# Kernel optimization log

Measured on AMD Instinct MI355X. Metric: run time of the kernel, lower is better.

The kernel has to match this reference:

```python
import jax, jax.numpy as jnp
import numpy as np

MAP_CHANNEL_WEIGHT = 50.0
PATCH = 3  # unfold kernel size and stride (stride == kernel -> non-overlapping)


def setup_inputs() -> dict:
    key = jax.random.key(0)
    k1, k2, k3, k4 = jax.random.split(key, 4)
    style_resp = jax.random.normal(k1, (1, 256, 256, 256), dtype=jnp.float32)
    style_map = jax.random.uniform(k2, (1, 3, 1024, 1024), dtype=jnp.float32)
    output_map = jax.random.uniform(k3, (1, 3, 1024, 1024), dtype=jnp.float32)
    model_resp = jax.random.normal(k4, (1, 256, 256, 256), dtype=jnp.float32)
    return {"style_resp": style_resp, "style_map": style_map,
            "output_map": output_map, "model_resp": model_resp}


def _avg_pool(x, d):
    # x: (N, C, H, W) -> AvgPool2d((d, d)) with default stride = kernel
    n, c, h, w = x.shape
    return x.reshape(n, c, h // d, d, w // d, d).mean(axis=(3, 5))


def _unfold(x):
    # x: (C, H, W) -> (C*3*3, P) matching torch.nn.Unfold((3,3), stride=3)
    # block layout along dim 0 is (C, kh, kw); patches are row-major.
    c, h, w = x.shape
    nh = (h - PATCH) // PATCH + 1
    nw = (w - PATCH) // PATCH + 1
    x = x[:, : nh * PATCH, : nw * PATCH].reshape(c, nh, PATCH, nw, PATCH)
    x = x.transpose(0, 2, 4, 1, 3)  # (C, kh, kw, nh, nw)
    return x.reshape(c * PATCH * PATCH, nh * nw)


def reference(style_resp, style_map, output_map, model_resp):
    # --- init-time precomputation (faithful to __init__) ---
    channel_count = style_resp.shape[0]  # original code uses dim 0 (batch) here
    patch_height = style_resp.shape[2]
    down = style_map.shape[2] // patch_height
    style_map_down = _avg_pool(style_map, down)
    output_map_down = _avg_pool(output_map, down)
    sr = jnp.concatenate(
        [style_resp, MAP_CHANNEL_WEIGHT * style_map_down * channel_count], axis=1)
    style_patches = _unfold(sr[0])                      # (D, P)
    style_norm_inv = 1.0 / jnp.linalg.norm(style_patches, axis=0)  # (P,)

    # --- loss(model_response) ---
    img = jnp.concatenate(
        [model_resp, MAP_CHANNEL_WEIGHT * output_map_down * channel_count], axis=1)
    img_patches = _unfold(img[0])                       # (D, P)
    img_norm_inv = 1.0 / jnp.linalg.norm(img_patches, axis=0)      # (P,)

    # Faithful to original: sim = ((img^T @ style) * img_norm[j]).T * style_norm[j]
    # => C[i, j] = <img_j, style_i> * img_norm_inv[i] * style_norm_inv[j]
    sim = jnp.einsum('di,dj->ij', style_patches, img_patches)  # (P, P): <style_i, img_j>
    sim = sim * img_norm_inv[:, None] * style_norm_inv[None, :]
    nearest = jnp.argmax(sim, axis=1)                   # (P,)

    matched = style_patches[:, nearest]                 # (D, P)
    loss = jnp.mean((img_patches - matched) ** 2)
    return loss
```

## Files before the change

kernel.cpp:

```cpp
#include <hip/hip_runtime.h>
#include <float.h>
#include <math.h>

#define D_REAL 2331
#define D_PAD  2336
#define DQ     2304
#define N_REAL 7225
#define N_PAD  7296
#define JTILES 57
#define ITILES 57
#define STILES 15

typedef __attribute__((ext_vector_type(8))) short bf16x8_t;
typedef __attribute__((ext_vector_type(4))) float f32x4_t;
typedef __attribute__((ext_vector_type(8))) int   v8i_t;
typedef __attribute__((ext_vector_type(4))) int   v4i_t;

__device__ __forceinline__ unsigned short f2bf(float x) {
    union { float f; unsigned int u; } v; v.f = x;
    unsigned int r = v.u + 0x7FFFu + ((v.u >> 16) & 1u);
    return (unsigned short)(r >> 16);
}
__device__ __forceinline__ float bflo(unsigned int u) {
    union { unsigned int x; float f; } v; v.x = u << 16; return v.f;
}
__device__ __forceinline__ float bfhi(unsigned int u) {
    union { unsigned int x; float f; } v; v.x = u & 0xFFFF0000u; return v.f;
}

#define GLOAD_LDS16(g, l) __builtin_amdgcn_global_load_lds( \
    (const __attribute__((address_space(1))) void*)(g),     \
    (__attribute__((address_space(3))) void*)(l), 16, 0, 0)

__global__ __launch_bounds__(256) void build_all(
        const float* __restrict__ respS, const float* __restrict__ respI,
        const float* __restrict__ mapS,  const float* __restrict__ mapI,
        unsigned short* __restrict__ PbS, unsigned short* __restrict__ PbI,
        unsigned char* __restrict__ PqS, unsigned char* __restrict__ PqI) {
    const int mat = blockIdx.y;
    unsigned short* Pb = mat ? PbI : PbS;
    const int bx = blockIdx.x;
    if (bx < 6120) {
        const float* resp = mat ? respI : respS;
        unsigned char* Pq = mat ? PqI : PqS;
        __shared__ float slab[5 * 768];
        const int u  = bx / 72;
        const int d0 = (bx - u * 72) * 32;
        const int c0 = d0 / 9;
        const int cN = (d0 + 31) / 9 - c0 + 1;
        const int total4 = cN * 192;
        for (int idx = threadIdx.x; idx < total4; idx += 256) {
            int cc = idx / 192;
            int rem = idx - cc * 192;
            *(float4*)&slab[cc * 768 + rem * 4] =
                *(const float4*)&resp[(((size_t)(c0 + cc)) << 16)
                                      + ((size_t)(3 * u) << 8) + rem * 4];
        }
        __syncthreads();
        const int dl16 = threadIdx.x & 15;
        const int de = d0 + 2 * dl16, dq = de + 1;
        const int ce = de / 9, re = de - ce * 9, pe = re / 3, qe = re - pe * 3;
        const int co = dq / 9, ro = dq - co * 9, po = ro / 3, qo = ro - po * 3;
        const int base_e = (ce - c0) * 768 + pe * 256 + qe;
        const int base_o = (co - c0) * 768 + po * 256 + qo;
        const int v0 = threadIdx.x >> 4;
        for (int v = v0; v < 85; v += 16) {
            float x0 = slab[base_e + 3 * v];
            float x1 = slab[base_o + 3 * v];
            size_t row = (size_t)(u * 85 + v);
            *(unsigned int*)&Pb[row * D_PAD + de] =
                (unsigned int)f2bf(x0) | ((unsigned int)f2bf(x1) << 16);
            int pk = __builtin_amdgcn_cvt_pk_fp8_f32(x0, x1, 0, false);
            *(unsigned short*)&Pq[row * DQ + de] = (unsigned short)pk;
        }
    } else {
        const float* map = mat ? mapI : mapS;
        int t = (bx - 6120) * 256 + threadIdx.x;
        int n = t >> 5, dm = t & 31;
        if (n >= N_REAL) return;
        float val = 0.f;
        if (dm < 27) {
            int u = n / 85, v = n - u * 85;
            int ch = dm / 9, r9 = dm - ch * 9, p = r9 / 3, q = r9 - p * 3;
            const float* mp = map + ((size_t)ch << 20)
                                  + ((size_t)((3 * u + p) * 4) << 10)
                                  + (size_t)((3 * v + q) * 4);
            float s = 0.f;
            #pragma unroll
            for (int a = 0; a < 4; a++)
                #pragma unroll
                for (int b = 0; b < 4; b++) s += mp[a * 1024 + b];
            val = 3.125f * s;
        }
        Pb[(size_t)n * D_PAD + 2304 + dm] = f2bf(val);
    }
}

__global__ __launch_bounds__(256) void col_norms(const unsigned short* __restrict__ Sb,
                                                 float* __restrict__ sinv) {
    int n = blockIdx.x * 4 + (threadIdx.x >> 6);
    int lane = threadIdx.x & 63;
    const uint4* sp = (const uint4*)(Sb + (size_t)n * D_PAD);
    float s = 0.f;
    for (int k = lane; k < D_PAD / 8; k += 64) {
        uint4 a = sp[k];
        float x0 = bflo(a.x), x1 = bfhi(a.x), x2 = bflo(a.y), x3 = bfhi(a.y);
        float x4 = bflo(a.z), x5 = bfhi(a.z), x6 = bflo(a.w), x7 = bfhi(a.w);
        s = fmaf(x0, x0, s); s = fmaf(x1, x1, s);
        s = fmaf(x2, x2, s); s = fmaf(x3, x3, s);
        s = fmaf(x4, x4, s); s = fmaf(x5, x5, s);
        s = fmaf(x6, x6, s); s = fmaf(x7, x7, s);
    }
    #pragma unroll
    for (int off = 32; off > 0; off >>= 1) s += __shfl_xor(s, off);
    if (lane == 0) sinv[n] = (n < N_REAL) ? rsqrtf(s) : 0.f;
}

__global__ __launch_bounds__(256) void gemm_argmax(
        const unsigned char* __restrict__ Sq, const unsigned char* __restrict__ Iq,
        const unsigned short* __restrict__ Sb, const unsigned short* __restrict__ Ib,
        const float* __restrict__ sinv,
        float* __restrict__ pval, int* __restrict__ pidx) {
    const int lb = blockIdx.x;
    const int sup = lb >> 4, win = lb & 15;
    const int it4 = (sup / STILES) * 4 + (win & 3);
    const int jt4 = (sup % STILES) * 4 + (win >> 2);
    if (it4 >= ITILES || jt4 >= JTILES) return;
    const int i0 = it4 * 128, j0 = jt4 * 128;

    __shared__ __align__(16) unsigned char Af[2][128][128];
    __shared__ __align__(16) unsigned char Bf[2][128][128];
    const int tid = threadIdx.x;
    const int L = tid & 63, w = tid >> 6;
    const int m = L & 15, q = L >> 4;
    const int wi = (w >> 1) * 64, wj = (w & 1) * 64;

    f32x4_t acc[4][4];
    #pragma unroll
    for (int a = 0; a < 4; a++)
        #pragma unroll
        for (int b = 0; b < 4; b++) acc[a][b] = (f32x4_t){0.f, 0.f, 0.f, 0.f};

    const int rl = L >> 3;
    const int ck = (L & 7) ^ rl;
    const unsigned char* gqa = Sq + (size_t)(i0 + w * 32 + rl) * DQ + (ck << 4);
    const unsigned char* gqb = Iq + (size_t)(j0 + w * 32 + rl) * DQ + (ck << 4);

    const int clo = ((((q << 1))     ^ (m & 7)) << 4);
    const int chi = ((((q << 1) | 1) ^ (m & 7)) << 4);

    unsigned short (*At)[32] = (unsigned short(*)[32])&Af[0][0][0];
    unsigned short (*Bt)[32] = (unsigned short(*)[32])&Bf[0][0][0];
    const int rl2 = L >> 2;
    const int ck2 = (L & 3) ^ ((rl2 >> 1) & 3);
    const unsigned short* gta = Sb + (size_t)(i0 + w * 32 + rl2) * D_PAD + 2304 + (ck2 << 3);
    const unsigned short* gtb = Ib + (size_t)(j0 + w * 32 + rl2) * D_PAD + 2304 + (ck2 << 3);
    const int cht = (q ^ ((m >> 1) & 3)) << 3;

#define PREFETCH_Q(buf) {                                     \
    GLOAD_LDS16(gqa,             &Af[buf][w * 32     ][0]);   \
    GLOAD_LDS16(gqa +  8 * DQ,   &Af[buf][w * 32 +  8][0]);   \
    GLOAD_LDS16(gqa + 16 * DQ,   &Af[buf][w * 32 + 16][0]);   \
    GLOAD_LDS16(gqa + 24 * DQ,   &Af[buf][w * 32 + 24][0]);   \
    GLOAD_LDS16(gqb,             &Bf[buf][w * 32     ][0]);   \
    GLOAD_LDS16(gqb +  8 * DQ,   &Bf[buf][w * 32 +  8][0]);   \
    GLOAD_LDS16(gqb + 16 * DQ,   &Bf[buf][w * 32 + 16][0]);   \
    GLOAD_LDS16(gqb + 24 * DQ,   &Bf[buf][w * 32 + 24][0]);   \
    gqa += 128; gqb += 128; }

#define COMPUTE_Q(buf) {                                                   \
    v8i_t aq[4], bq[4];                                                    \
    _Pragma("unroll")                                                      \
    for (int mi = 0; mi < 4; mi++) {                                       \
        v4i_t lo = *(const v4i_t*)&Af[buf][wi + mi * 16 + m][clo];         \
        v4i_t hi = *(const v4i_t*)&Af[buf][wi + mi * 16 + m][chi];         \
        aq[mi] = __builtin_shufflevector(lo, hi, 0, 1, 2, 3, 4, 5, 6, 7);  \
    }                                                                      \
    _Pragma("unroll")                                                      \
    for (int nj = 0; nj < 4; nj++) {                                       \
        v4i_t lo = *(const v4i_t*)&Bf[buf][wj + nj * 16 + m][clo];         \
        v4i_t hi = *(const v4i_t*)&Bf[buf][wj + nj * 16 + m][chi];         \
        bq[nj] = __builtin_shufflevector(lo, hi, 0, 1, 2, 3, 4, 5, 6, 7);  \
    }                                                                      \
    _Pragma("unroll")                                                      \
    for (int mi = 0; mi < 4; mi++)                                         \
        _Pragma("unroll")                                                  \
        for (int nj = 0; nj < 4; nj++)                                     \
            acc[mi][nj] = __builtin_amdgcn_mfma_scale_f32_16x16x128_f8f6f4(\
                aq[mi], bq[nj], acc[mi][nj], 0, 0, 0, 0x7F, 0, 0x7F); }

    PREFETCH_Q(0)
    for (int p = 0; p < 8; p++) {
        __syncthreads();
        PREFETCH_Q(1)
        __builtin_amdgcn_sched_barrier(0);
        COMPUTE_Q(0)
        __syncthreads();
        PREFETCH_Q(0)
        __builtin_amdgcn_sched_barrier(0);
        COMPUTE_Q(1)
    }
    __syncthreads();
    PREFETCH_Q(1)
    __builtin_amdgcn_sched_barrier(0);
    COMPUTE_Q(0)
    __syncthreads();
    {
        GLOAD_LDS16(gta,                      &At[w * 32][0]);
        GLOAD_LDS16(gta + (size_t)16 * D_PAD, &At[w * 32 + 16][0]);
        GLOAD_LDS16(gtb,                      &Bt[w * 32][0]);
        GLOAD_LDS16(gtb + (size_t)16 * D_PAD, &Bt[w * 32 + 16][0]);
    }
    __builtin_amdgcn_sched_barrier(0);
    COMPUTE_Q(1)
    __syncthreads();
    {
        bf16x8_t af[4], bfr[4];
        #pragma unroll
        for (int mi = 0; mi < 4; mi++)
            af[mi] = *(const bf16x8_t*)&At[wi + mi * 16 + m][cht];
        #pragma unroll
        for (int nj = 0; nj < 4; nj++)
            bfr[nj] = *(const bf16x8_t*)&Bt[wj + nj * 16 + m][cht];
        #pragma unroll
        for (int mi = 0; mi < 4; mi++)
            #pragma unroll
            for (int nj = 0; nj < 4; nj++)
                acc[mi][nj] = __builtin_amdgcn_mfma_f32_16x16x32_bf16(
                    af[mi], bfr[nj], acc[mi][nj], 0, 0, 0);
    }
#undef PREFETCH_Q
#undef COMPUTE_Q

    float sjv[4];
    #pragma unroll
    for (int nj = 0; nj < 4; nj++) sjv[nj] = sinv[j0 + wj + nj * 16 + m];
    #pragma unroll
    for (int mi = 0; mi < 4; mi++) {
        #pragma unroll
        for (int r = 0; r < 4; r++) {
            float best = -INFINITY; int bidx = 0x7fffffff;
            #pragma unroll
            for (int nj = 0; nj < 4; nj++) {
                int j = j0 + wj + nj * 16 + m;
                float v = (j < N_REAL) ? acc[mi][nj][r] * sjv[nj] : -INFINITY;
                if (v > best) { best = v; bidx = j; }
            }
            #pragma unroll
            for (int off = 1; off < 16; off <<= 1) {
                float ov = __shfl_xor(best, off);
                int   oi = __shfl_xor(bidx, off);
                if (ov > best || (ov == best && oi < bidx)) { best = ov; bidx = oi; }
            }
            if (m == 0) {
                int i = i0 + wi + mi * 16 + q * 4 + r;
                pval[(size_t)jt4 * N_PAD + i] = best;
                pidx[(size_t)jt4 * N_PAD + i] = bidx;
            }
        }
    }
}

__global__ __launch_bounds__(256) void loss_kernel(
        const unsigned short* __restrict__ Ib, const unsigned short* __restrict__ Sb,
        const float* __restrict__ pval, const int* __restrict__ pidx,
        double* __restrict__ partial) {
    __shared__ float wsum[4];
    __shared__ int sjn;
    const int n = blockIdx.x;
    if (threadIdx.x < 64) {
        float v = -INFINITY; int id = 0x7fffffff;
        if (threadIdx.x < JTILES) {
            v  = pval[(size_t)threadIdx.x * N_PAD + n];
            id = pidx[(size_t)threadIdx.x * N_PAD + n];
        }
        #pragma unroll
        for (int off = 32; off > 0; off >>= 1) {
            float ov = __shfl_xor(v, off);
            int   oi = __shfl_xor(id, off);
            if (ov > v || (ov == v && oi < id)) { v = ov; id = oi; }
        }
        if (threadIdx.x == 0) sjn = id;
    }
    __syncthreads();
    const int jn = sjn;
    const uint4* ip = (const uint4*)(Ib + (size_t)n  * D_PAD);
    const uint4* sp = (const uint4*)(Sb + (size_t)jn * D_PAD);
    float s = 0.f;
    for (int k = threadIdx.x; k < D_PAD / 8; k += 256) {
        uint4 a = ip[k], b = sp[k];
        float d0 = bflo(a.x) - bflo(b.x), d1 = bfhi(a.x) - bfhi(b.x);
        float d2 = bflo(a.y) - bflo(b.y), d3 = bfhi(a.y) - bfhi(b.y);
        float d4 = bflo(a.z) - bflo(b.z), d5 = bfhi(a.z) - bfhi(b.z);
        float d6 = bflo(a.w) - bflo(b.w), d7 = bfhi(a.w) - bfhi(b.w);
        s = fmaf(d0, d0, s); s = fmaf(d1, d1, s);
        s = fmaf(d2, d2, s); s = fmaf(d3, d3, s);
        s = fmaf(d4, d4, s); s = fmaf(d5, d5, s);
        s = fmaf(d6, d6, s); s = fmaf(d7, d7, s);
    }
    #pragma unroll
    for (int off = 32; off > 0; off >>= 1) s += __shfl_xor(s, off);
    int lane = threadIdx.x & 63, wv = threadIdx.x >> 6;
    if (lane == 0) wsum[wv] = s;
    __syncthreads();
    if (threadIdx.x == 0) {
        partial[n] = (double)wsum[0] + (double)wsum[1]
                   + (double)wsum[2] + (double)wsum[3];
    }
}

__global__ __launch_bounds__(256) void finalize(const double* __restrict__ partial,
                                                float* __restrict__ out) {
    __shared__ double ws[4];
    double s = 0.0;
    for (int i = threadIdx.x; i < N_REAL; i += 256) s += partial[i];
    #pragma unroll
    for (int off = 32; off > 0; off >>= 1) s += __shfl_xor(s, off);
    int lane = threadIdx.x & 63, wv = threadIdx.x >> 6;
    if (lane == 0) ws[wv] = s;
    __syncthreads();
    if (threadIdx.x == 0) {
        double t = ws[0] + ws[1] + ws[2] + ws[3];
        out[0] = (float)(t / (double)((long long)D_REAL * N_REAL));
    }
}

extern "C" void kernel_launch(void* const* d_in, const int* in_sizes, int n_in,
                              void* d_out, int out_size, void* d_ws, size_t ws_size,
                              hipStream_t stream) {
    const float* style_resp = (const float*)d_in[0];
    const float* style_map  = (const float*)d_in[1];
    const float* output_map = (const float*)d_in[2];
    const float* model_resp = (const float*)d_in[3];
    float* out = (float*)d_out;

    unsigned short* Sb = (unsigned short*)d_ws;
    unsigned short* Ib = Sb + (size_t)D_PAD * N_PAD;
    unsigned char*  Sq = (unsigned char*)(Ib + (size_t)D_PAD * N_PAD);
    unsigned char*  Iq = Sq + (size_t)DQ * N_PAD;
    float* sinv     = (float*)(Iq + (size_t)DQ * N_PAD);
    float* pval     = sinv + N_PAD;
    int*   pidx     = (int*)(pval + (size_t)JTILES * N_PAD);
    double* partial = (double*)(pidx + (size_t)JTILES * N_PAD);

    build_all<<<dim3(6120 + 904, 2), 256, 0, stream>>>(
        style_resp, model_resp, style_map, output_map, Sb, Ib, Sq, Iq);

    col_norms<<<N_PAD / 4, 256, 0, stream>>>(Sb, sinv);

    gemm_argmax<<<STILES * STILES * 16, 256, 0, stream>>>(Sq, Iq, Sb, Ib, sinv, pval, pidx);

    loss_kernel<<<N_REAL, 256, 0, stream>>>(Ib, Sb, pval, pidx, partial);
    finalize<<<1, 256, 0, stream>>>(partial, out);
}
```

Baseline: 425.0 us.

## Load fp8 A operand directly into registers, halve LDS, target two blocks per CU

The style-patch (A) operand of the fp8 GEMM is now loaded straight from global memory into registers in MFMA fragment layout, double-buffered in registers, and no longer staged through shared memory. Only B goes through LDS, which halves LDS use, and launch bounds now ask for two blocks per CU. The map pooling loop also switches to float4 loads. The trade-off is more register pressure, plus A fragment loads that are less coalesced, with each lane reading 32 bytes from separate rows and no cross-wave reuse of A.

```diff
diff --git a/kernel.cpp b/kernel.cpp
--- a/kernel.cpp
+++ b/kernel.cpp
@@ -87,9 +87,10 @@
                                   + (size_t)((3 * v + q) * 4);
             float s = 0.f;
             #pragma unroll
-            for (int a = 0; a < 4; a++)
-                #pragma unroll
-                for (int b = 0; b < 4; b++) s += mp[a * 1024 + b];
+            for (int a = 0; a < 4; a++) {
+                float4 r = *(const float4*)(mp + a * 1024);
+                s += (r.x + r.y) + (r.z + r.w);
+            }
             val = 3.125f * s;
         }
         Pb[(size_t)n * D_PAD + 2304 + dm] = f2bf(val);
@@ -116,7 +117,7 @@
     if (lane == 0) sinv[n] = (n < N_REAL) ? rsqrtf(s) : 0.f;
 }
 
-__global__ __launch_bounds__(256) void gemm_argmax(
+__global__ __launch_bounds__(256, 2) void gemm_argmax(
         const unsigned char* __restrict__ Sq, const unsigned char* __restrict__ Iq,
         const unsigned short* __restrict__ Sb, const unsigned short* __restrict__ Ib,
         const float* __restrict__ sinv,
@@ -128,7 +129,6 @@
     if (it4 >= ITILES || jt4 >= JTILES) return;
     const int i0 = it4 * 128, j0 = jt4 * 128;
 
-    __shared__ __align__(16) unsigned char Af[2][128][128];
     __shared__ __align__(16) unsigned char Bf[2][128][128];
     const int tid = threadIdx.x;
     const int L = tid & 63, w = tid >> 6;
@@ -143,39 +143,43 @@
 
     const int rl = L >> 3;
     const int ck = (L & 7) ^ rl;
-    const unsigned char* gqa = Sq + (size_t)(i0 + w * 32 + rl) * DQ + (ck << 4);
     const unsigned char* gqb = Iq + (size_t)(j0 + w * 32 + rl) * DQ + (ck << 4);
 
     const int clo = ((((q << 1))     ^ (m & 7)) << 4);
     const int chi = ((((q << 1) | 1) ^ (m & 7)) << 4);
 
-    unsigned short (*At)[32] = (unsigned short(*)[32])&Af[0][0][0];
-    unsigned short (*Bt)[32] = (unsigned short(*)[32])&Bf[0][0][0];
+    const unsigned char* gA[4];
+    #pragma unroll
+    for (int mi = 0; mi < 4; mi++)
+        gA[mi] = Sq + (size_t)(i0 + wi + mi * 16 + m) * DQ + (q << 5);
+
+    unsigned short (*At)[32] = (unsigned short(*)[32])&Bf[0][0][0];
+    unsigned short (*Bt)[32] = (unsigned short(*)[32])&Bf[0][64][0];
     const int rl2 = L >> 2;
     const int ck2 = (L & 3) ^ ((rl2 >> 1) & 3);
     const unsigned short* gta = Sb + (size_t)(i0 + w * 32 + rl2) * D_PAD + 2304 + (ck2 << 3);
     const unsigned short* gtb = Ib + (size_t)(j0 + w * 32 + rl2) * D_PAD + 2304 + (ck2 << 3);
     const int cht = (q ^ ((m >> 1) & 3)) << 3;
 
-#define PREFETCH_Q(buf) {                                     \
-    GLOAD_LDS16(gqa,             &Af[buf][w * 32     ][0]);   \
-    GLOAD_LDS16(gqa +  8 * DQ,   &Af[buf][w * 32 +  8][0]);   \
-    GLOAD_LDS16(gqa + 16 * DQ,   &Af[buf][w * 32 + 16][0]);   \
-    GLOAD_LDS16(gqa + 24 * DQ,   &Af[buf][w * 32 + 24][0]);   \
+    v4i_t A0[8], A1[8];
+
+#define LOADA(Ar) {                                           \
+    _Pragma("unroll")                                         \
+    for (int mi = 0; mi < 4; mi++) {                          \
+        Ar[2 * mi]     = *(const v4i_t*)(gA[mi]);             \
+        Ar[2 * mi + 1] = *(const v4i_t*)(gA[mi] + 16);        \
+        gA[mi] += 128;                                        \
+    } }
+
+#define PREFETCH_B(buf) {                                     \
     GLOAD_LDS16(gqb,             &Bf[buf][w * 32     ][0]);   \
     GLOAD_LDS16(gqb +  8 * DQ,   &Bf[buf][w * 32 +  8][0]);   \
     GLOAD_LDS16(gqb + 16 * DQ,   &Bf[buf][w * 32 + 16][0]);   \
     GLOAD_LDS16(gqb + 24 * DQ,   &Bf[buf][w * 32 + 24][0]);   \
-    gqa += 128; gqb += 128; }
-
-#define COMPUTE_Q(buf) {                                                   \
-    v8i_t aq[4], bq[4];                                                    \
-    _Pragma("unroll")                                                      \
-    for (int mi = 0; mi < 4; mi++) {                                       \
-        v4i_t lo = *(const v4i_t*)&Af[buf][wi + mi * 16 + m][clo];         \
-        v4i_t hi = *(const v4i_t*)&Af[buf][wi + mi * 16 + m][chi];         \
-        aq[mi] = __builtin_shufflevector(lo, hi, 0, 1, 2, 3, 4, 5, 6, 7);  \
-    }                                                                      \
+    gqb += 128; }
+
+#define COMPUTE_Q(buf, Ar) {                                               \
+    v8i_t bq[4];                                                           \
     _Pragma("unroll")                                                      \
     for (int nj = 0; nj < 4; nj++) {                                       \
         v4i_t lo = *(const v4i_t*)&Bf[buf][wj + nj * 16 + m][clo];         \
@@ -183,27 +187,34 @@
         bq[nj] = __builtin_shufflevector(lo, hi, 0, 1, 2, 3, 4, 5, 6, 7);  \
     }                                                                      \
     _Pragma("unroll")                                                      \
-    for (int mi = 0; mi < 4; mi++)                                         \
+    for (int mi = 0; mi < 4; mi++) {                                       \
+        v8i_t aq = __builtin_shufflevector(Ar[2 * mi], Ar[2 * mi + 1],     \
+                                           0, 1, 2, 3, 4, 5, 6, 7);        \
         _Pragma("unroll")                                                  \
         for (int nj = 0; nj < 4; nj++)                                     \
             acc[mi][nj] = __builtin_amdgcn_mfma_scale_f32_16x16x128_f8f6f4(\
-                aq[mi], bq[nj], acc[mi][nj], 0, 0, 0, 0x7F, 0, 0x7F); }
-
-    PREFETCH_Q(0)
+                aq, bq[nj], acc[mi][nj], 0, 0, 0, 0x7F, 0, 0x7F);          \
+    } }
+
+    LOADA(A0)
+    PREFETCH_B(0)
     for (int p = 0; p < 8; p++) {
         __syncthreads();
-        PREFETCH_Q(1)
+        LOADA(A1)
+        PREFETCH_B(1)
         __builtin_amdgcn_sched_barrier(0);
-        COMPUTE_Q(0)
+        COMPUTE_Q(0, A0)
         __syncthreads();
-        PREFETCH_Q(0)
+        LOADA(A0)
+        PREFETCH_B(0)
         __builtin_amdgcn_sched_barrier(0);
-        COMPUTE_Q(1)
-    }
-    __syncthreads();
-    PREFETCH_Q(1)
+        COMPUTE_Q(1, A1)
+    }
+    __syncthreads();
+    LOADA(A1)
+    PREFETCH_B(1)
     __builtin_amdgcn_sched_barrier(0);
-    COMPUTE_Q(0)
+    COMPUTE_Q(0, A0)
     __syncthreads();
     {
         GLOAD_LDS16(gta,                      &At[w * 32][0]);
@@ -212,7 +223,7 @@
         GLOAD_LDS16(gtb + (size_t)16 * D_PAD, &Bt[w * 32 + 16][0]);
     }
     __builtin_amdgcn_sched_barrier(0);
-    COMPUTE_Q(1)
+    COMPUTE_Q(1, A1)
     __syncthreads();
     {
         bf16x8_t af[4], bfr[4];
@@ -229,7 +240,8 @@
                 acc[mi][nj] = __builtin_amdgcn_mfma_f32_16x16x32_bf16(
                     af[mi], bfr[nj], acc[mi][nj], 0, 0, 0);
     }
-#undef PREFETCH_Q
+#undef LOADA
+#undef PREFETCH_B
 #undef COMPUTE_Q
 
     float sjv[4];
```

New measurement: 540.2 us. +27.1%, slower.
